# Optimization experiments

Hardware: AMD Instinct MI355X
Metric: run time of the kernel (lower is better)

## Reference

```python
import jax, jax.numpy as jnp
import numpy as np

B, T, C, H = 4, 2048, 1024, 16
HS = C // H
DFF = 4 * C
EPS = 1e-5


def setup_inputs() -> dict:
    key = jax.random.key(0)
    ks = jax.random.split(key, 8)
    s = 0.02
    inp = {
        "x": jax.random.normal(ks[0], (B, T, C), jnp.float32),
        # attention linear weights, stored (in, out) so h @ W + b
        "Wq": jax.random.normal(ks[1], (C, C), jnp.float32) * s,
        "bq": jnp.zeros((C,), jnp.float32),
        "Wk": jax.random.normal(ks[2], (C, C), jnp.float32) * s,
        "bk": jnp.zeros((C,), jnp.float32),
        "Wv": jax.random.normal(ks[3], (C, C), jnp.float32) * s,
        "bv": jnp.zeros((C,), jnp.float32),
        "Wo": jax.random.normal(ks[4], (C, C), jnp.float32) * s,
        "bo": jnp.zeros((C,), jnp.float32),
        # feed-forward
        "W1": jax.random.normal(ks[5], (C, DFF), jnp.float32) * s,
        "b1": jnp.zeros((DFF,), jnp.float32),
        "W2": jax.random.normal(ks[6], (DFF, C), jnp.float32) * s,
        "b2": jnp.zeros((C,), jnp.float32),
        # layernorms
        "g1": jnp.ones((C,), jnp.float32),
        "be1": jnp.zeros((C,), jnp.float32),
        "g2": jnp.ones((C,), jnp.float32),
        "be2": jnp.zeros((C,), jnp.float32),
    }
    return inp


def _layernorm(x, g, b):
    mu = jnp.mean(x, axis=-1, keepdims=True)
    var = jnp.mean(jnp.square(x - mu), axis=-1, keepdims=True)
    return (x - mu) * jax.lax.rsqrt(var + EPS) * g + b


def _attention(h, Wq, bq, Wk, bk, Wv, bv, Wo, bo):
    Bx, Tx, Cx = h.shape
    q = (h @ Wq + bq).reshape(Bx, Tx, H, HS).transpose(0, 2, 1, 3)  # [B,H,T,hs]
    k = (h @ Wk + bk).reshape(Bx, Tx, H, HS).transpose(0, 2, 1, 3)
    v = (h @ Wv + bv).reshape(Bx, Tx, H, HS).transpose(0, 2, 1, 3)
    att = jnp.einsum("bhqd,bhkd->bhqk", q, k) * (1.0 / np.sqrt(HS))
    causal = jnp.tril(jnp.ones((Tx, Tx), bool))
    att = jnp.where(causal, att, jnp.float32(-jnp.inf))
    att = jax.nn.softmax(att, axis=-1)
    y = jnp.einsum("bhqk,bhkd->bhqd", att, v)
    y = y.transpose(0, 2, 1, 3).reshape(Bx, Tx, Cx)
    return y @ Wo + bo


def reference(x, Wq, bq, Wk, bk, Wv, bv, Wo, bo, W1, b1, W2, b2, g1, be1, g2, be2):
    x = x + _attention(_layernorm(x, g1, be1), Wq, bq, Wk, bk, Wv, bv, Wo, bo)
    h = _layernorm(x, g2, be2)
    ff = jax.nn.relu(h @ W1 + b1) @ W2 + b2
    return x + ff
```

## Files before the change

kernel.cpp:

```cpp
#include <hip/hip_runtime.h>
#include <hip/hip_bf16.h>

#define Bq   4
#define Tq   2048
#define Cq   1024
#define Hq   16
#define HSq  64
#define DFFq 4096
#define Mq   (Bq*Tq)

typedef float f32x4  __attribute__((ext_vector_type(4)));
typedef short bf16x8 __attribute__((ext_vector_type(8)));

__device__ __forceinline__ float b2f(unsigned short u){ return __uint_as_float(((unsigned)u)<<16); }
__device__ __forceinline__ unsigned short f2b(float f){
  union { __hip_bfloat16 h; unsigned short u; } cv;
  cv.h = __float2bfloat16(f);
  return cv.u;
}

__device__ __forceinline__ void gld_lds16(const unsigned short* g, unsigned short* l){
  __builtin_amdgcn_global_load_lds(
      (const __attribute__((address_space(1))) void*)g,
      (__attribute__((address_space(3))) void*)l, 16, 0, 0);
}

__global__ void detect_k(const unsigned short* __restrict__ w, int* __restrict__ flag){
  if (threadIdx.x==0 && blockIdx.x==0){
    int cnt=0;
    for (int i=0;i<256;i++){
      const unsigned e = (w[i]>>7)&0xFF;
      cnt += (e>=0x60 && e<=0x7E) ? 1 : 0;
    }
    *flag = (cnt>=224) ? 1 : 0;
  }
}

__global__ __launch_bounds__(256) void cvtvec_k(
    const void* s0,const void* s1,const void* s2,const void* s3,const void* s4,
    const void* s5,const void* s6,const void* s7,const void* s8,const void* s9,
    const int* __restrict__ flag, unsigned short* __restrict__ dst)
{
  const int idx = blockIdx.x*256 + threadIdx.x;
  const int seg = idx>>12, off = idx&4095;
  const void* s; int len;
  switch(seg){
    case 0: s=s0; len=1024; break;
    case 1: s=s1; len=1024; break;
    case 2: s=s2; len=1024; break;
    case 3: s=s3; len=1024; break;
    case 4: s=s4; len=4096; break;
    case 5: s=s5; len=1024; break;
    case 6: s=s6; len=1024; break;
    case 7: s=s7; len=1024; break;
    case 8: s=s8; len=1024; break;
    default: s=s9; len=1024; break;
  }
  if (off >= len) return;
  const float v = (*flag) ? b2f(((const unsigned short*)s)[off]) : ((const float*)s)[off];
  dst[idx] = f2b(v);
}

__global__ __launch_bounds__(256) void ln_k(const void* __restrict__ xin,
    const unsigned short* __restrict__ g, const unsigned short* __restrict__ be,
    unsigned short* __restrict__ out, const int* __restrict__ flag)
{
  const int row = blockIdx.x;
  const int tid = threadIdx.x;
  const int isbf = *flag;
  float v[4];
  if (isbf){
    const unsigned short* xr = (const unsigned short*)xin + (size_t)row*Cq;
    ushort4 u = *(const ushort4*)(xr + tid*4);
    v[0]=b2f(u.x); v[1]=b2f(u.y); v[2]=b2f(u.z); v[3]=b2f(u.w);
  } else {
    const float* xr = (const float*)xin + (size_t)row*Cq;
    float4 u = *(const float4*)(xr + tid*4);
    v[0]=u.x; v[1]=u.y; v[2]=u.z; v[3]=u.w;
  }
  float s  = v[0]+v[1]+v[2]+v[3];
  float ss = v[0]*v[0]+v[1]*v[1]+v[2]*v[2]+v[3]*v[3];
#pragma unroll
  for (int off=32; off>0; off>>=1){
    s  += __shfl_down(s,  off, 64);
    ss += __shfl_down(ss, off, 64);
  }
  __shared__ float sa[4], sb[4];
  const int wave = tid>>6, lane = tid&63;
  if (lane==0){ sa[wave]=s; sb[wave]=ss; }
  __syncthreads();
  s  = sa[0]+sa[1]+sa[2]+sa[3];
  ss = sb[0]+sb[1]+sb[2]+sb[3];
  const float mu  = s  * (1.0f/Cq);
  const float var = ss * (1.0f/Cq) - mu*mu;
  const float rs  = rsqrtf(fmaxf(var, 0.0f) + 1e-5f);
  ushort4 o; unsigned short* op = (unsigned short*)&o;
#pragma unroll
  for (int i=0;i<4;i++){
    const int ci = tid*4+i;
    op[i] = f2b((v[i]-mu)*rs*b2f(g[ci]) + b2f(be[ci]));
  }
  *(ushort4*)(out + (size_t)row*Cq + tid*4) = o;
}

__global__ __launch_bounds__(256) void wtrans_k(const void* __restrict__ Win,
    unsigned short* __restrict__ Wt, const int Kd, const int Nd,
    const int* __restrict__ flag)
{
  __shared__ __align__(16) unsigned short tile[64][72];
  const int kb = blockIdx.x, nb = blockIdx.y, tid = threadIdx.x;
  const int isbf = *flag;
#pragma unroll
  for (int i=0;i<2;i++){
    const int v = tid + i*256;
    const int kr = v>>3, nc = (v&7)*8;
    if (isbf){
      *(uint4*)&tile[kr][nc] =
        *(const uint4*)((const unsigned short*)Win + (size_t)(kb*64+kr)*Nd + nb*64 + nc);
    } else {
      const float* wp = (const float*)Win + (size_t)(kb*64+kr)*Nd + nb*64 + nc;
      float4 a = *(const float4*)wp, b = *(const float4*)(wp+4);
      alignas(16) unsigned short t[8] =
        {f2b(a.x),f2b(a.y),f2b(a.z),f2b(a.w),f2b(b.x),f2b(b.y),f2b(b.z),f2b(b.w)};
      *(uint4*)&tile[kr][nc] = *(const uint4*)t;
    }
  }
  __syncthreads();
#pragma unroll
  for (int i=0;i<2;i++){
    const int v = tid + i*256;
    const int nr = v>>3, kc = (v&7)*8;
    alignas(16) unsigned short tmp[8];
#pragma unroll
    for (int j=0;j<8;j++) tmp[j] = tile[kc+j][nr];
    *(uint4*)(Wt + (size_t)(nb*64+nr)*Kd + kb*64 + kc) = *(const uint4*)tmp;
  }
}

template<int RELU, int RES, int OUTV, int EXTIO>
__global__ __launch_bounds__(256,2) void gemm_bt(
    const unsigned short* __restrict__ A,
    const unsigned short* __restrict__ Bt,
    const unsigned short* __restrict__ bias,
    const void* resid, void* outp,
    const int N, const int K, const int* flag)
{
  __shared__ __align__(16) unsigned short Al[128][64];
  __shared__ __align__(16) unsigned short Bl[128][64];
  const int tid  = threadIdx.x;
  const int lane = tid & 63, wave = tid >> 6;
  const int qd   = lane >> 4, c = lane & 15;
  const int m0   = blockIdx.x * 128, n0 = blockIdx.y * 128;
  const int wm   = (wave & 1) * 64, wn = (wave >> 1) * 64;
  const int srow = tid >> 3, scol = (tid & 7) * 8;
  const int isbf = EXTIO ? *flag : 1;

  const f32x4 zf = {0.f,0.f,0.f,0.f};
  f32x4 acc[4][4];
#pragma unroll
  for (int i=0;i<4;i++)
#pragma unroll
    for (int j=0;j<4;j++) acc[i][j] = zf;

  const int kTiles = K >> 6;
  for (int kt=0; kt<kTiles; ++kt){
    const int k0 = kt*64;
#pragma unroll
    for (int i=0;i<4;i++){
      const int row = i*32 + srow;
      gld_lds16(A  + (size_t)(m0+row)*K + k0 + scol, &Al[row][scol]);
      gld_lds16(Bt + (size_t)(n0+row)*K + k0 + scol, &Bl[row][scol]);
    }
    __syncthreads();
#pragma unroll
    for (int ks=0; ks<2; ++ks){
      bf16x8 af[4], bfr[4];
#pragma unroll
      for (int mt=0;mt<4;mt++) af[mt]  = *(const bf16x8*)&Al[wm+mt*16+c][ks*32+qd*8];
#pragma unroll
      for (int nt=0;nt<4;nt++) bfr[nt] = *(const bf16x8*)&Bl[wn+nt*16+c][ks*32+qd*8];
#pragma unroll
      for (int mt=0;mt<4;mt++)
#pragma unroll
        for (int nt=0;nt<4;nt++)
          acc[mt][nt] = __builtin_amdgcn_mfma_f32_16x16x32_bf16(af[mt], bfr[nt], acc[mt][nt], 0,0,0);
    }
    __syncthreads();
  }

  float bv[4];
#pragma unroll
  for (int nt=0;nt<4;nt++) bv[nt] = b2f(bias[n0+wn+nt*16+c]);
#pragma unroll
  for (int mt=0;mt<4;mt++){
#pragma unroll
    for (int r=0;r<4;r++){
      const int m = m0 + wm + mt*16 + qd*4 + r;
#pragma unroll
      for (int nt=0;nt<4;nt++){
        const int n = n0 + wn + nt*16 + c;
        const size_t idx = (size_t)m*N + n;
        float val = acc[mt][nt][r] + bv[nt];
        if (RELU) val = fmaxf(val, 0.0f);
        if (RES){
          if (EXTIO && !isbf) val += ((const float*)resid)[idx];
          else                val += b2f(((const unsigned short*)resid)[idx]);
        }
        if (OUTV){
          const size_t vidx = ((size_t)((m>>11)*16 + (n>>6))*64 + (n&63))*Tq + (m&2047);
          ((unsigned short*)outp)[vidx] = f2b(val);
        } else if (EXTIO && !isbf){
          ((float*)outp)[idx] = val;
        } else {
          ((unsigned short*)outp)[idx] = f2b(val);
        }
      }
    }
  }
}

__global__ __launch_bounds__(256,3) void attn_k(const unsigned short* __restrict__ Qg,
    const unsigned short* __restrict__ Kg, const unsigned short* __restrict__ Vt,
    unsigned short* __restrict__ Y)
{
  const int bh = blockIdx.x;
  const int jq = (int)(gridDim.y - 1) - blockIdx.y;
  const int b = bh >> 4, h = bh & 15;
  const int tid = threadIdx.x, lane = tid & 63, wave = tid >> 6;
  const int qd = lane >> 4, c = lane & 15;
  const int q0  = jq * 128;
  const int wq0 = q0 + wave * 32;
  __shared__ __align__(16) unsigned short Kl[64*64];
  __shared__ __align__(16) unsigned short Vl[64*64];
  __shared__ __align__(16) unsigned short Pl[4][32][72];

  bf16x8 qf[2][2];
#pragma unroll
  for (int nt=0; nt<2; ++nt)
#pragma unroll
    for (int h2=0; h2<2; ++h2)
      qf[nt][h2] = *(const bf16x8*)(Qg + ((size_t)b*Tq + wq0 + nt*16 + c)*Cq
                                       + h*HSq + h2*32 + qd*8);

  const f32x4 zf = {0.f,0.f,0.f,0.f};
  const float NEG = -1.0e30f;
  f32x4 o[2][4];
  float m_[2] = {NEG, NEG}, l_[2] = {0.f, 0.f};
#pragma unroll
  for (int nt=0;nt<2;nt++)
#pragma unroll
    for (int dt=0;dt<4;dt++) o[nt][dt]=zf;
  const float SCL = 0.125f * 1.44269504088896340736f;

  const int stg_r  = (lane>>3);
  const int stg_pg = lane & 7;

  const int nkt = 2*(jq+1);
  for (int kt=0; kt<nkt; ++kt){
    const int k0 = kt*64;
#pragma unroll
    for (int i=0;i<2;i++){
      const int r  = (wave*2+i)*8 + stg_r;
      const int lg = (stg_pg + r) & 7;
      gld_lds16(Kg + ((size_t)b*Tq + k0 + r)*Cq + h*HSq + lg*8,
                &Kl[r*64 + stg_pg*8]);
      gld_lds16(Vt + ((size_t)bh*HSq + r)*Tq + k0 + lg*8,
                &Vl[r*64 + stg_pg*8]);
    }
    __syncthreads();

    if (k0 <= wq0 + 31){
      bf16x8 kf[4][2], vf[4][2];
#pragma unroll
      for (int mt=0;mt<4;mt++)
#pragma unroll
        for (int h2=0;h2<2;h2++){
          kf[mt][h2] = *(const bf16x8*)&Kl[(mt*16+c)*64 + ((h2*4+qd-c)&7)*8];
          vf[mt][h2] = *(const bf16x8*)&Vl[(mt*16+c)*64 + ((h2*4+qd-c)&7)*8];
        }
      const int domask = (k0 + 63 > wq0) ? 1 : 0;
#pragma unroll
      for (int nt=0; nt<2; ++nt){
        const int query = wq0 + nt*16 + c;
        f32x4 s[4];
#pragma unroll
        for (int mt=0;mt<4;mt++){
          f32x4 sa = zf;
          sa = __builtin_amdgcn_mfma_f32_16x16x32_bf16(kf[mt][0], qf[nt][0], sa, 0,0,0);
          sa = __builtin_amdgcn_mfma_f32_16x16x32_bf16(kf[mt][1], qf[nt][1], sa, 0,0,0);
          s[mt] = sa;
        }
        float sv[4][4];
#pragma unroll
        for (int mt=0;mt<4;mt++)
#pragma unroll
          for (int r=0;r<4;r++){
            float x = s[mt][r]*SCL;
            if (domask && (k0 + mt*16 + qd*4 + r > query)) x = NEG;
            sv[mt][r] = x;
          }
        float mx = NEG;
#pragma unroll
        for (int mt=0;mt<4;mt++)
#pragma unroll
          for (int r=0;r<4;r++) mx = fmaxf(mx, sv[mt][r]);
        mx = fmaxf(mx, __shfl_xor(mx, 16, 64));
        mx = fmaxf(mx, __shfl_xor(mx, 32, 64));
        const float mnew = fmaxf(m_[nt], mx);
        const float al   = exp2f(m_[nt] - mnew);
        m_[nt] = mnew;
        float rs = 0.f;
        alignas(8) unsigned short pw[4];
#pragma unroll
        for (int mt=0;mt<4;mt++){
#pragma unroll
          for (int r=0;r<4;r++){
            const float p = exp2f(sv[mt][r] - mnew);
            rs += p;
            pw[r] = f2b(p);
          }
          *(uint2*)&Pl[wave][nt*16+c][mt*16+qd*4] = *(const uint2*)pw;
        }
        rs += __shfl_xor(rs, 16, 64);
        rs += __shfl_xor(rs, 32, 64);
        l_[nt] = l_[nt]*al + rs;
#pragma unroll
        for (int dt=0;dt<4;dt++){
          f32x4 t = o[nt][dt];
          t[0]*=al; t[1]*=al; t[2]*=al; t[3]*=al;
          o[nt][dt] = t;
        }
        bf16x8 pf0 = *(const bf16x8*)&Pl[wave][nt*16+c][qd*8];
        bf16x8 pf1 = *(const bf16x8*)&Pl[wave][nt*16+c][32+qd*8];
#pragma unroll
        for (int dt=0;dt<4;dt++){
          o[nt][dt] = __builtin_amdgcn_mfma_f32_16x16x32_bf16(vf[dt][0], pf0, o[nt][dt], 0,0,0);
          o[nt][dt] = __builtin_amdgcn_mfma_f32_16x16x32_bf16(vf[dt][1], pf1, o[nt][dt], 0,0,0);
        }
      }
    }
    __syncthreads();
  }

#pragma unroll
  for (int nt=0;nt<2;nt++){
    const float inv = 1.0f / l_[nt];
    alignas(8) unsigned short ow[4];
#pragma unroll
    for (int dt=0;dt<4;dt++){
#pragma unroll
      for (int r=0;r<4;r++) ow[r] = f2b(o[nt][dt][r]*inv);
      *(uint2*)&Pl[wave][nt*16+c][dt*16+qd*4] = *(const uint2*)ow;
    }
  }
#pragma unroll
  for (int pass=0; pass<4; ++pass){
    const int qrow = pass*8 + (lane>>3);
    const int dcol = (lane&7)*8;
    uint4 val = *(const uint4*)&Pl[wave][qrow][dcol];
    *(uint4*)(Y + ((size_t)b*Tq + wq0 + qrow)*Cq + h*HSq + dcol) = val;
  }
}

extern "C" void kernel_launch(void* const* d_in, const int* in_sizes, int n_in,
                              void* d_out, int out_size, void* d_ws, size_t ws_size,
                              hipStream_t stream)
{
  (void)in_sizes; (void)n_in; (void)out_size; (void)ws_size;
  const void* x   = d_in[0];
  const void* Wq  = d_in[1];
  const void* Wk  = d_in[3];
  const void* Wv  = d_in[5];
  const void* Wo  = d_in[7];
  const void* W1  = d_in[9];
  const void* W2  = d_in[11];

  char* ws = (char*)d_ws;
  const size_t MB = 1u<<20;
  unsigned short* W1T = (unsigned short*)(ws + 0*MB);
  unsigned short* W2T = (unsigned short*)(ws + 8*MB);
  unsigned short* WqT = (unsigned short*)(ws + 16*MB);
  unsigned short* WkT = (unsigned short*)(ws + 18*MB);
  unsigned short* WvT = (unsigned short*)(ws + 20*MB);
  unsigned short* WoT = (unsigned short*)(ws + 22*MB);
  unsigned short* Qb  = (unsigned short*)(ws + 24*MB);
  unsigned short* Kb  = (unsigned short*)(ws + 40*MB);
  unsigned short* Vt  = (unsigned short*)(ws + 56*MB);
  unsigned short* ff1 = (unsigned short*)(ws + 16*MB);
  unsigned short* hy  = (unsigned short*)(ws + 80*MB);
  int*            flg = (int*)(ws + 96*MB);
  unsigned short* vec = (unsigned short*)(ws + 96*MB + 65536);
  unsigned short* vbq = vec;          unsigned short* vbk = vec + 4096;
  unsigned short* vbv = vec + 8192;   unsigned short* vbo = vec + 12288;
  unsigned short* vb1 = vec + 16384;  unsigned short* vb2 = vec + 20480;
  unsigned short* vg1 = vec + 24576;  unsigned short* vbe1= vec + 28672;
  unsigned short* vg2 = vec + 32768;  unsigned short* vbe2= vec + 36864;

  const dim3 blk(256,1,1);

  detect_k<<<dim3(1), dim3(64), 0, stream>>>((const unsigned short*)W1, flg);
  cvtvec_k<<<dim3(160), blk, 0, stream>>>(d_in[2], d_in[4], d_in[6], d_in[8],
      d_in[10], d_in[12], d_in[13], d_in[14], d_in[15], d_in[16], flg, vec);

  wtrans_k<<<dim3(16,16), blk, 0, stream>>>(Wq, WqT, 1024, 1024, flg);
  wtrans_k<<<dim3(16,16), blk, 0, stream>>>(Wk, WkT, 1024, 1024, flg);
  wtrans_k<<<dim3(16,16), blk, 0, stream>>>(Wv, WvT, 1024, 1024, flg);
  wtrans_k<<<dim3(16,16), blk, 0, stream>>>(Wo, WoT, 1024, 1024, flg);
  wtrans_k<<<dim3(16,64), blk, 0, stream>>>(W1, W1T, 1024, 4096, flg);
  wtrans_k<<<dim3(64,16), blk, 0, stream>>>(W2, W2T, 4096, 1024, flg);

  ln_k<<<dim3(Mq), blk, 0, stream>>>(x, vg1, vbe1, hy, flg);

  gemm_bt<0,0,0,0><<<dim3(64,8), blk, 0, stream>>>(hy, WqT, vbq, nullptr, Qb, 1024, 1024, flg);
  gemm_bt<0,0,0,0><<<dim3(64,8), blk, 0, stream>>>(hy, WkT, vbk, nullptr, Kb, 1024, 1024, flg);
  gemm_bt<0,0,1,0><<<dim3(64,8), blk, 0, stream>>>(hy, WvT, vbv, nullptr, Vt, 1024, 1024, flg);

  attn_k<<<dim3(64,16), blk, 0, stream>>>(Qb, Kb, Vt, hy);

  gemm_bt<0,1,0,1><<<dim3(64,8), blk, 0, stream>>>(hy, WoT, vbo, x, d_out, 1024, 1024, flg);

  ln_k<<<dim3(Mq), blk, 0, stream>>>(d_out, vg2, vbe2, hy, flg);

  gemm_bt<1,0,0,0><<<dim3(64,32), blk, 0, stream>>>(hy,  W1T, vb1, nullptr, ff1, 4096, 1024, flg);
  gemm_bt<0,1,0,1><<<dim3(64,8),  blk, 0, stream>>>(ff1, W2T, vb2, d_out, d_out, 1024, 4096, flg);
}
```

Measured before the change: 588.5 us.

## Fuse QKV GEMMs, swizzle LDS tiles, split-K FFN2, inline dtype probe

Q, K and V now come from a single GEMM over a concatenated transposed weight, and the four attention weight transposes run in one launch. The global-to-LDS loads use an XOR-style swizzle to cut LDS bank conflicts on fragment reads. The FFN down-projection is split along K into two z-slices that accumulate into the output with float atomics when the input is fp32. The separate dtype-detect kernel is removed and every kernel probes the weights inline instead. The trade-offs are redundant probe work in every block and nondeterministic atomic accumulation order.

```diff
diff --git a/kernel.cpp b/kernel.cpp
--- a/kernel.cpp
+++ b/kernel.cpp
@@ -25,22 +25,28 @@
       (__attribute__((address_space(3))) void*)l, 16, 0, 0);
 }
 
-__global__ void detect_k(const unsigned short* __restrict__ w, int* __restrict__ flag){
-  if (threadIdx.x==0 && blockIdx.x==0){
-    int cnt=0;
-    for (int i=0;i<256;i++){
-      const unsigned e = (w[i]>>7)&0xFF;
-      cnt += (e>=0x60 && e<=0x7E) ? 1 : 0;
-    }
-    *flag = (cnt>=224) ? 1 : 0;
-  }
+__device__ __forceinline__ int probe_bf16(const unsigned short* w){
+  const int lane = threadIdx.x & 63;
+  ushort4 u = *(const ushort4*)(w + lane*4);
+  int cnt = 0;
+  {
+    unsigned e;
+    e=(u.x>>7)&0xFF; cnt += (e>=0x60 && e<=0x7E);
+    e=(u.y>>7)&0xFF; cnt += (e>=0x60 && e<=0x7E);
+    e=(u.z>>7)&0xFF; cnt += (e>=0x60 && e<=0x7E);
+    e=(u.w>>7)&0xFF; cnt += (e>=0x60 && e<=0x7E);
+  }
+#pragma unroll
+  for (int off=1; off<64; off<<=1) cnt += __shfl_xor(cnt, off, 64);
+  return cnt >= 224;
 }
 
 __global__ __launch_bounds__(256) void cvtvec_k(
     const void* s0,const void* s1,const void* s2,const void* s3,const void* s4,
     const void* s5,const void* s6,const void* s7,const void* s8,const void* s9,
-    const int* __restrict__ flag, unsigned short* __restrict__ dst)
-{
+    const unsigned short* __restrict__ probew, unsigned short* __restrict__ dst)
+{
+  const int isbf = probe_bf16(probew);
   const int idx = blockIdx.x*256 + threadIdx.x;
   const int seg = idx>>12, off = idx&4095;
   const void* s; int len;
@@ -57,17 +63,17 @@
     default: s=s9; len=1024; break;
   }
   if (off >= len) return;
-  const float v = (*flag) ? b2f(((const unsigned short*)s)[off]) : ((const float*)s)[off];
+  const float v = isbf ? b2f(((const unsigned short*)s)[off]) : ((const float*)s)[off];
   dst[idx] = f2b(v);
 }
 
 __global__ __launch_bounds__(256) void ln_k(const void* __restrict__ xin,
     const unsigned short* __restrict__ g, const unsigned short* __restrict__ be,
-    unsigned short* __restrict__ out, const int* __restrict__ flag)
-{
+    unsigned short* __restrict__ out, const unsigned short* __restrict__ probew)
+{
+  const int isbf = probe_bf16(probew);
   const int row = blockIdx.x;
   const int tid = threadIdx.x;
-  const int isbf = *flag;
   float v[4];
   if (isbf){
     const unsigned short* xr = (const unsigned short*)xin + (size_t)row*Cq;
@@ -103,13 +109,52 @@
   *(ushort4*)(out + (size_t)row*Cq + tid*4) = o;
 }
 
+__global__ __launch_bounds__(256) void wtrans4_k(
+    const void* __restrict__ w0, const void* __restrict__ w1,
+    const void* __restrict__ w2, const void* __restrict__ w3,
+    unsigned short* __restrict__ Wqkv, unsigned short* __restrict__ WoT,
+    const unsigned short* __restrict__ probew)
+{
+  const int isbf = probe_bf16(probew);
+  const int z = blockIdx.z;
+  const void* Win = (z==0)?w0 : (z==1)?w1 : (z==2)?w2 : w3;
+  unsigned short* Wt = (z<3) ? (Wqkv + (size_t)z*1048576) : WoT;
+  __shared__ __align__(16) unsigned short tile[64][72];
+  const int kb = blockIdx.x, nb = blockIdx.y, tid = threadIdx.x;
+#pragma unroll
+  for (int i=0;i<2;i++){
+    const int v = tid + i*256;
+    const int kr = v>>3, nc = (v&7)*8;
+    if (isbf){
+      *(uint4*)&tile[kr][nc] =
+        *(const uint4*)((const unsigned short*)Win + (size_t)(kb*64+kr)*1024 + nb*64 + nc);
+    } else {
+      const float* wp = (const float*)Win + (size_t)(kb*64+kr)*1024 + nb*64 + nc;
+      float4 a = *(const float4*)wp, b = *(const float4*)(wp+4);
+      alignas(16) unsigned short t[8] =
+        {f2b(a.x),f2b(a.y),f2b(a.z),f2b(a.w),f2b(b.x),f2b(b.y),f2b(b.z),f2b(b.w)};
+      *(uint4*)&tile[kr][nc] = *(const uint4*)t;
+    }
+  }
+  __syncthreads();
+#pragma unroll
+  for (int i=0;i<2;i++){
+    const int v = tid + i*256;
+    const int nr = v>>3, kc = (v&7)*8;
+    alignas(16) unsigned short tmp[8];
+#pragma unroll
+    for (int j=0;j<8;j++) tmp[j] = tile[kc+j][nr];
+    *(uint4*)(Wt + (size_t)(nb*64+nr)*1024 + kb*64 + kc) = *(const uint4*)tmp;
+  }
+}
+
 __global__ __launch_bounds__(256) void wtrans_k(const void* __restrict__ Win,
     unsigned short* __restrict__ Wt, const int Kd, const int Nd,
-    const int* __restrict__ flag)
-{
+    const unsigned short* __restrict__ probew)
+{
+  const int isbf = probe_bf16(probew);
   __shared__ __align__(16) unsigned short tile[64][72];
   const int kb = blockIdx.x, nb = blockIdx.y, tid = threadIdx.x;
-  const int isbf = *flag;
 #pragma unroll
   for (int i=0;i<2;i++){
     const int v = tid + i*256;
@@ -137,14 +182,29 @@
   }
 }
 
-template<int RELU, int RES, int OUTV, int EXTIO>
+template<int RELU, int RESMODE, int OUTMODE>
 __global__ __launch_bounds__(256,2) void gemm_bt(
     const unsigned short* __restrict__ A,
     const unsigned short* __restrict__ Bt,
     const unsigned short* __restrict__ bias,
     const void* resid, void* outp,
-    const int N, const int K, const int* flag)
-{
+    const int N, const int K, const int lda, const int ldb,
+    const unsigned short* __restrict__ probew)
+{
+  int isbf = 1;
+  if constexpr (OUTMODE==1 || OUTMODE==5 || RESMODE==2) isbf = probe_bf16(probew);
+
+  int koff = 0;
+  int kTiles = K >> 6;
+  if constexpr (OUTMODE==5){
+    if (isbf){
+      if (blockIdx.z) return;
+      kTiles = K >> 5;
+    } else {
+      koff = blockIdx.z * K;
+    }
+  }
+
   __shared__ __align__(16) unsigned short Al[128][64];
   __shared__ __align__(16) unsigned short Bl[128][64];
   const int tid  = threadIdx.x;
@@ -152,8 +212,8 @@
   const int qd   = lane >> 4, c = lane & 15;
   const int m0   = blockIdx.x * 128, n0 = blockIdx.y * 128;
   const int wm   = (wave & 1) * 64, wn = (wave >> 1) * 64;
-  const int srow = tid >> 3, scol = (tid & 7) * 8;
-  const int isbf = EXTIO ? *flag : 1;
+  const int srow = tid >> 3;
+  const int pg   = tid & 7;
 
   const f32x4 zf = {0.f,0.f,0.f,0.f};
   f32x4 acc[4][4];
@@ -162,23 +222,24 @@
 #pragma unroll
     for (int j=0;j<4;j++) acc[i][j] = zf;
 
-  const int kTiles = K >> 6;
   for (int kt=0; kt<kTiles; ++kt){
-    const int k0 = kt*64;
+    const int k0 = koff + kt*64;
 #pragma unroll
     for (int i=0;i<4;i++){
       const int row = i*32 + srow;
-      gld_lds16(A  + (size_t)(m0+row)*K + k0 + scol, &Al[row][scol]);
-      gld_lds16(Bt + (size_t)(n0+row)*K + k0 + scol, &Bl[row][scol]);
+      const int lg  = (pg + row) & 7;
+      gld_lds16(A  + (size_t)(m0+row)*lda + k0 + lg*8, &Al[row][pg*8]);
+      gld_lds16(Bt + (size_t)(n0+row)*ldb + k0 + lg*8, &Bl[row][pg*8]);
     }
     __syncthreads();
 #pragma unroll
     for (int ks=0; ks<2; ++ks){
+      const int rg = ((ks*4+qd-c)&7)*8;
       bf16x8 af[4], bfr[4];
 #pragma unroll
-      for (int mt=0;mt<4;mt++) af[mt]  = *(const bf16x8*)&Al[wm+mt*16+c][ks*32+qd*8];
-#pragma unroll
-      for (int nt=0;nt<4;nt++) bfr[nt] = *(const bf16x8*)&Bl[wn+nt*16+c][ks*32+qd*8];
+      for (int mt=0;mt<4;mt++) af[mt]  = *(const bf16x8*)&Al[wm+mt*16+c][rg];
+#pragma unroll
+      for (int nt=0;nt<4;nt++) bfr[nt] = *(const bf16x8*)&Bl[wn+nt*16+c][rg];
 #pragma unroll
       for (int mt=0;mt<4;mt++)
 #pragma unroll
@@ -189,8 +250,16 @@
   }
 
   float bv[4];
-#pragma unroll
-  for (int nt=0;nt<4;nt++) bv[nt] = b2f(bias[n0+wn+nt*16+c]);
+  if constexpr (OUTMODE==3){
+    const int segn = (n0+wn) >> 10;
+    const unsigned short* bseg = bias + segn*4096;
+#pragma unroll
+    for (int nt=0;nt<4;nt++) bv[nt] = b2f(bseg[(n0+wn+nt*16+c)&1023]);
+  } else {
+#pragma unroll
+    for (int nt=0;nt<4;nt++) bv[nt] = b2f(bias[n0+wn+nt*16+c]);
+  }
+
 #pragma unroll
   for (int mt=0;mt<4;mt++){
 #pragma unroll
@@ -199,20 +268,37 @@
 #pragma unroll
       for (int nt=0;nt<4;nt++){
         const int n = n0 + wn + nt*16 + c;
-        const size_t idx = (size_t)m*N + n;
-        float val = acc[mt][nt][r] + bv[nt];
+        float val = acc[mt][nt][r] + ((OUTMODE==5 && !isbf && blockIdx.z!=0) ? 0.0f : bv[nt]);
         if (RELU) val = fmaxf(val, 0.0f);
-        if (RES){
-          if (EXTIO && !isbf) val += ((const float*)resid)[idx];
-          else                val += b2f(((const unsigned short*)resid)[idx]);
-        }
-        if (OUTV){
-          const size_t vidx = ((size_t)((m>>11)*16 + (n>>6))*64 + (n&63))*Tq + (m&2047);
-          ((unsigned short*)outp)[vidx] = f2b(val);
-        } else if (EXTIO && !isbf){
-          ((float*)outp)[idx] = val;
+        if constexpr (RESMODE==2){
+          const size_t idx = (size_t)m*N + n;
+          val += isbf ? b2f(((const unsigned short*)resid)[idx])
+                      : ((const float*)resid)[idx];
+        }
+        if constexpr (OUTMODE==3){
+          const int segn = (n0+wn) >> 10;
+          const int n1 = n & 1023;
+          unsigned short* dst = (unsigned short*)outp + (size_t)segn*8388608;
+          if (segn < 2){
+            dst[(size_t)m*1024 + n1] = f2b(val);
+          } else {
+            const size_t vidx = ((size_t)((m>>11)*16 + (n1>>6))*64 + (n1&63))*Tq + (m&2047);
+            dst[vidx] = f2b(val);
+          }
+        } else if constexpr (OUTMODE==5){
+          const size_t idx = (size_t)m*N + n;
+          if (!isbf){
+            atomicAdd((float*)outp + idx, val);
+          } else {
+            unsigned short* o16 = (unsigned short*)outp;
+            o16[idx] = f2b(val + b2f(o16[idx]));
+          }
+        } else if constexpr (OUTMODE==1){
+          const size_t idx = (size_t)m*N + n;
+          if (isbf) ((unsigned short*)outp)[idx] = f2b(val);
+          else      ((float*)outp)[idx] = val;
         } else {
-          ((unsigned short*)outp)[idx] = f2b(val);
+          ((unsigned short*)outp)[(size_t)m*N + n] = f2b(val);
         }
       }
     }
@@ -374,53 +460,48 @@
   const void* Wo  = d_in[7];
   const void* W1  = d_in[9];
   const void* W2  = d_in[11];
+  const unsigned short* pw = (const unsigned short*)W1;
 
   char* ws = (char*)d_ws;
   const size_t MB = 1u<<20;
-  unsigned short* W1T = (unsigned short*)(ws + 0*MB);
-  unsigned short* W2T = (unsigned short*)(ws + 8*MB);
-  unsigned short* WqT = (unsigned short*)(ws + 16*MB);
-  unsigned short* WkT = (unsigned short*)(ws + 18*MB);
-  unsigned short* WvT = (unsigned short*)(ws + 20*MB);
-  unsigned short* WoT = (unsigned short*)(ws + 22*MB);
-  unsigned short* Qb  = (unsigned short*)(ws + 24*MB);
-  unsigned short* Kb  = (unsigned short*)(ws + 40*MB);
-  unsigned short* Vt  = (unsigned short*)(ws + 56*MB);
-  unsigned short* ff1 = (unsigned short*)(ws + 16*MB);
-  unsigned short* hy  = (unsigned short*)(ws + 80*MB);
-  int*            flg = (int*)(ws + 96*MB);
-  unsigned short* vec = (unsigned short*)(ws + 96*MB + 65536);
-  unsigned short* vbq = vec;          unsigned short* vbk = vec + 4096;
-  unsigned short* vbv = vec + 8192;   unsigned short* vbo = vec + 12288;
+  unsigned short* W1T   = (unsigned short*)(ws + 0*MB);
+  unsigned short* W2T   = (unsigned short*)(ws + 8*MB);
+  unsigned short* WqkvT = (unsigned short*)(ws + 16*MB);
+  unsigned short* WoT   = (unsigned short*)(ws + 22*MB);
+  unsigned short* Qb    = (unsigned short*)(ws + 24*MB);
+  unsigned short* Kb    = (unsigned short*)(ws + 40*MB);
+  unsigned short* Vt    = (unsigned short*)(ws + 56*MB);
+  unsigned short* ff1   = (unsigned short*)(ws + 16*MB);
+  unsigned short* hy    = (unsigned short*)(ws + 80*MB);
+  unsigned short* vec   = (unsigned short*)(ws + 96*MB);
+  unsigned short* vbo = vec + 12288;
   unsigned short* vb1 = vec + 16384;  unsigned short* vb2 = vec + 20480;
   unsigned short* vg1 = vec + 24576;  unsigned short* vbe1= vec + 28672;
   unsigned short* vg2 = vec + 32768;  unsigned short* vbe2= vec + 36864;
 
   const dim3 blk(256,1,1);
 
-  detect_k<<<dim3(1), dim3(64), 0, stream>>>((const unsigned short*)W1, flg);
   cvtvec_k<<<dim3(160), blk, 0, stream>>>(d_in[2], d_in[4], d_in[6], d_in[8],
-      d_in[10], d_in[12], d_in[13], d_in[14], d_in[15], d_in[16], flg, vec);
-
-  wtrans_k<<<dim3(16,16), blk, 0, stream>>>(Wq, WqT, 1024, 1024, flg);
-  wtrans_k<<<dim3(16,16), blk, 0, stream>>>(Wk, WkT, 1024, 1024, flg);
-  wtrans_k<<<dim3(16,16), blk, 0, stream>>>(Wv, WvT, 1024, 1024, flg);
-  wtrans_k<<<dim3(16,16), blk, 0, stream>>>(Wo, WoT, 1024, 1024, flg);
-  wtrans_k<<<dim3(16,64), blk, 0, stream>>>(W1, W1T, 1024, 4096, flg);
-  wtrans_k<<<dim3(64,16), blk, 0, stream>>>(W2, W2T, 4096, 1024, flg);
-
-  ln_k<<<dim3(Mq), blk, 0, stream>>>(x, vg1, vbe1, hy, flg);
-
-  gemm_bt<0,0,0,0><<<dim3(64,8), blk, 0, stream>>>(hy, WqT, vbq, nullptr, Qb, 1024, 1024, flg);
-  gemm_bt<0,0,0,0><<<dim3(64,8), blk, 0, stream>>>(hy, WkT, vbk, nullptr, Kb, 1024, 1024, flg);
-  gemm_bt<0,0,1,0><<<dim3(64,8), blk, 0, stream>>>(hy, WvT, vbv, nullptr, Vt, 1024, 1024, flg);
+      d_in[10], d_in[12], d_in[13], d_in[14], d_in[15], d_in[16], pw, vec);
+
+  wtrans4_k<<<dim3(16,16,4), blk, 0, stream>>>(Wq, Wk, Wv, Wo, WqkvT, WoT, pw);
+  wtrans_k<<<dim3(16,64), blk, 0, stream>>>(W1, W1T, 1024, 4096, pw);
+  wtrans_k<<<dim3(64,16), blk, 0, stream>>>(W2, W2T, 4096, 1024, pw);
+
+  ln_k<<<dim3(Mq), blk, 0, stream>>>(x, vg1, vbe1, hy, pw);
+
+  gemm_bt<0,0,3><<<dim3(64,24), blk, 0, stream>>>(hy, WqkvT, vec, nullptr, Qb,
+      3072, 1024, 1024, 1024, pw);
 
   attn_k<<<dim3(64,16), blk, 0, stream>>>(Qb, Kb, Vt, hy);
 
-  gemm_bt<0,1,0,1><<<dim3(64,8), blk, 0, stream>>>(hy, WoT, vbo, x, d_out, 1024, 1024, flg);
-
-  ln_k<<<dim3(Mq), blk, 0, stream>>>(d_out, vg2, vbe2, hy, flg);
-
-  gemm_bt<1,0,0,0><<<dim3(64,32), blk, 0, stream>>>(hy,  W1T, vb1, nullptr, ff1, 4096, 1024, flg);
-  gemm_bt<0,1,0,1><<<dim3(64,8),  blk, 0, stream>>>(ff1, W2T, vb2, d_out, d_out, 1024, 4096, flg);
-}
+  gemm_bt<0,2,1><<<dim3(64,8), blk, 0, stream>>>(hy, WoT, vbo, x, d_out,
+      1024, 1024, 1024, 1024, pw);
+
+  ln_k<<<dim3(Mq), blk, 0, stream>>>(d_out, vg2, vbe2, hy, pw);
+
+  gemm_bt<1,0,0><<<dim3(64,32), blk, 0, stream>>>(hy, W1T, vb1, nullptr, ff1,
+      4096, 1024, 1024, 1024, pw);
+  gemm_bt<0,0,5><<<dim3(64,8,2), blk, 0, stream>>>(ff1, W2T, vb2, nullptr, d_out,
+      1024, 2048, 4096, 4096, pw);
+}
```

After: 510.7 us. 13.2% less time.
